# Optimization experiments

Hardware: AMD Instinct MI355X
Metric: run time of the kernel (lower is better)

The kernel has to match this reference:

```python
import jax, jax.numpy as jnp
import numpy as np

B, T, E = 2, 2048, 1024
H = 16
D = E // H  # head_dim = 64


def setup_inputs() -> dict:
    key = jax.random.key(0)
    k1, k2, k3 = jax.random.split(key, 3)
    x = jax.random.normal(k1, (B, T, E), dtype=jnp.float32)
    w_qkv = jax.random.normal(k2, (3 * E, E), dtype=jnp.float32) * 0.02
    w_proj = jax.random.normal(k3, (E, E), dtype=jnp.float32) * 0.02
    return {"x": x, "w_qkv": w_qkv, "w_proj": w_proj}


def reference(x, w_qkv, w_proj):
    b, t, c = x.shape
    # qkv projection (torch Linear: x @ W^T), split into q,k,v
    qkv = jnp.einsum('btc,fc->btf', x, w_qkv)  # [B,T,3E]
    q, k, v = jnp.split(qkv, 3, axis=-1)
    # [B,T,E] -> [B,H,T,D]
    q = q.reshape(b, t, H, D).transpose(0, 2, 1, 3)
    k = k.reshape(b, t, H, D).transpose(0, 2, 1, 3)
    v = v.reshape(b, t, H, D).transpose(0, 2, 1, 3)
    scale = 1.0 / jnp.sqrt(jnp.float32(D))
    att = jnp.einsum('bhqd,bhkd->bhqk', q, k) * scale  # [B,H,T,T]
    causal = jnp.tril(jnp.ones((t, t), dtype=bool))
    att = jnp.where(causal[None, None], att, -jnp.inf)
    att = jax.nn.softmax(att, axis=-1)
    out = jnp.einsum('bhqk,bhkd->bhqd', att, v)  # [B,H,T,D]
    out = out.transpose(0, 2, 1, 3).reshape(b, t, c)  # [B,T,E]
    out = jnp.einsum('btc,oc->bto', out, w_proj)
    return out
```

## Files before the change

### kernel.cpp

```cpp
#include <hip/hip_runtime.h>
#include <stdint.h>
#include <stddef.h>

typedef __attribute__((ext_vector_type(8))) short s16x8;
typedef __attribute__((ext_vector_type(4))) short s16x4;
typedef __attribute__((ext_vector_type(4))) float f32x4;

#define B_  2
#define T_  2048
#define E_  1024
#define H_  16
#define E3_ 3072

__device__ __forceinline__ short f2bf(float f) {
  union { float f; uint32_t u; } v; v.f = f;
  uint32_t u = v.u;
  return (short)((u + 0x7FFFu + ((u >> 16) & 1u)) >> 16);
}

__device__ __forceinline__ uint32_t fbits(float f) {
  union { float f; uint32_t u; } v; v.f = f; return v.u;
}

__device__ __forceinline__ void gload_lds16(const short* g, short* l) {
  __builtin_amdgcn_global_load_lds(
      (__attribute__((address_space(1))) void*)(const_cast<short*>(g)),
      (__attribute__((address_space(3))) void*)(l), 16, 0, 0);
}

__global__ void castk_all(const float* __restrict__ x, const float* __restrict__ wqkv,
                          const float* __restrict__ wproj, short* __restrict__ xb,
                          short* __restrict__ wqkvb, short* __restrict__ wprojb) {
  const int bid = blockIdx.x;
  const float* in; short* out; int i; float sc = 1.0f;
  if (bid < 4096)      { in = x;     out = xb;     i = bid * 256 + threadIdx.x; }
  else if (bid < 7168) { in = wqkv;  out = wqkvb;  i = (bid - 4096) * 256 + threadIdx.x;
                         if (i < 262144) sc = 0.18033688011112042f; }
  else                 { in = wproj; out = wprojb; i = (bid - 7168) * 256 + threadIdx.x; }
  const float4 v = ((const float4*)in)[i];
  s16x4 o;
  o[0] = f2bf(v.x * sc); o[1] = f2bf(v.y * sc);
  o[2] = f2bf(v.z * sc); o[3] = f2bf(v.w * sc);
  ((s16x4*)out)[i] = o;
}

template <int MODE>
__global__ void gemm_nt_128(const short* __restrict__ A, const short* __restrict__ B,
                            void* __restrict__ Cv, short* __restrict__ vt,
                            int M, int N, int K) {
  __shared__ short As[128 * 32];
  __shared__ short Bs[128 * 32];
  const int tid  = threadIdx.x;
  const int lane = tid & 63;
  const int w    = tid >> 6;
  const int quad = lane >> 4;
  const int l16  = lane & 15;
  const int wm   = (w >> 1) * 64;
  const int wn   = (w & 1) * 64;
  const int bm   = blockIdx.y * 128;
  const int bn   = blockIdx.x * 128;

  f32x4 acc[4][4];
#pragma unroll
  for (int i = 0; i < 4; i++)
#pragma unroll
    for (int j = 0; j < 4; j++) acc[i][j] = (f32x4){0.f, 0.f, 0.f, 0.f};

  const int srow = w * 32 + (lane >> 2);
  const int scol = (lane & 3) * 8;
  const short* gA = A + (size_t)(bm + srow) * K + scol;
  const short* gB = B + (size_t)(bn + srow) * K + scol;
  short* lA = As + (w * 32) * 32;
  short* lB = Bs + (w * 32) * 32;

  for (int k0 = 0; k0 < K; k0 += 32) {
    __syncthreads();
    gload_lds16(gA + k0,          lA);
    gload_lds16(gA + 16 * K + k0, lA + 16 * 32);
    gload_lds16(gB + k0,          lB);
    gload_lds16(gB + 16 * K + k0, lB + 16 * 32);
    __syncthreads();

    s16x8 a[4], b[4];
#pragma unroll
    for (int i = 0; i < 4; i++)
      a[i] = *(const s16x8*)&As[(wm + i * 16 + l16) * 32 + quad * 8];
#pragma unroll
    for (int j = 0; j < 4; j++)
      b[j] = *(const s16x8*)&Bs[(wn + j * 16 + l16) * 32 + quad * 8];
#pragma unroll
    for (int i = 0; i < 4; i++)
#pragma unroll
      for (int j = 0; j < 4; j++)
        acc[i][j] = __builtin_amdgcn_mfma_f32_16x16x32_bf16(a[i], b[j], acc[i][j], 0, 0, 0);
  }

  if (MODE == 2 && bn >= 2 * E_) {
#pragma unroll
    for (int i = 0; i < 4; i++) {
      const int token = bm + wm + i * 16 + quad * 4;
      const int bb = token >> 11, t = token & (T_ - 1);
#pragma unroll
      for (int j = 0; j < 4; j++) {
        const int col = bn + wn + j * 16 + l16 - 2 * E_;
        s16x4 pk;
#pragma unroll
        for (int r = 0; r < 4; r++) pk[r] = f2bf(acc[i][j][r]);
        *(s16x4*)&vt[((size_t)(bb * H_ + (col >> 6)) * 64 + (col & 63)) * T_ + t] = pk;
      }
    }
  } else {
#pragma unroll
    for (int i = 0; i < 4; i++) {
      const int row0 = bm + wm + i * 16 + quad * 4;
#pragma unroll
      for (int j = 0; j < 4; j++) {
        const int col = bn + wn + j * 16 + l16;
#pragma unroll
        for (int r = 0; r < 4; r++) {
          const size_t idx = (size_t)(row0 + r) * N + col;
          if (MODE == 2) ((short*)Cv)[idx] = f2bf(acc[i][j][r]);
          else           ((float*)Cv)[idx] = acc[i][j][r];
        }
      }
    }
  }
}

__global__ void __launch_bounds__(128, 2)
attn_kernel(const short* __restrict__ qkv, const short* __restrict__ vt,
            short* __restrict__ attout) {
  __shared__ short Ks[2][64 * 64];
  __shared__ short Vs[2][64 * 64];
  __shared__ short Ps[2][32 * 64];
  const int tid  = threadIdx.x;
  const int lane = tid & 63;
  const int w    = tid >> 6;
  const int quad = lane >> 4;
  const int l16  = lane & 15;
  const int bh = blockIdx.x;
  const int b = bh >> 4, h = bh & 15;
  const int ya = blockIdx.y & 7, yb = blockIdx.y >> 3;
  const int qt = yb * 8 + ((yb & 1) ? (7 - ya) : ya);
  const int q0b = qt * 64;
  const float NEG_INF = -__builtin_inff();

  const int srl = lane >> 3;
  const int sgc = ((lane & 7) ^ srl) * 8;
  const short* gK = qkv + (size_t)(b * T_) * E3_ + E_ + h * 64 + sgc;
  const short* gV = vt + (size_t)(bh * 64) * T_ + sgc;
  const int swz = (l16 & 7);

  s16x8 ones;
#pragma unroll
  for (int i = 0; i < 8; i++) ones[i] = (short)0x3F80;

  auto stage = [&](int kv0s, int bf) {
#pragma unroll
    for (int i = 0; i < 4; i++) {
      const int row = w * 32 + i * 8 + srl;
      gload_lds16(gK + (size_t)(kv0s + row) * E3_, &Ks[bf][(w * 32 + i * 8) * 64]);
      gload_lds16(gV + (size_t)row * T_ + kv0s,    &Vs[bf][(w * 32 + i * 8) * 64]);
    }
  };

  s16x8 qf[2][2];
#pragma unroll
  for (int sub = 0; sub < 2; sub++) {
    const short* qbase = qkv + (size_t)(b * T_ + q0b + w * 32 + sub * 16 + l16) * E3_ + h * 64 + quad * 8;
    qf[sub][0] = *(const s16x8*)(qbase);
    qf[sub][1] = *(const s16x8*)(qbase + 32);
  }

  f32x4 o[2][4], ol[2];
#pragma unroll
  for (int sub = 0; sub < 2; sub++) {
    ol[sub] = (f32x4){0.f, 0.f, 0.f, 0.f};
#pragma unroll
    for (int j = 0; j < 4; j++) o[sub][j] = (f32x4){0.f, 0.f, 0.f, 0.f};
  }

  stage(0, 0);
  __syncthreads();

  for (int kv0 = 0, g = 0; kv0 <= q0b; kv0 += 64, g++) {
    const int cur = g & 1;

    if (kv0 + 64 <= q0b) stage(kv0 + 64, cur ^ 1);

    f32x4 s[2][4];
#pragma unroll
    for (int sub = 0; sub < 2; sub++)
#pragma unroll
      for (int j = 0; j < 4; j++) s[sub][j] = (f32x4){0.f, 0.f, 0.f, 0.f};

    __builtin_amdgcn_s_setprio(1);
#pragma unroll
    for (int c = 0; c < 2; c++) {
      s16x8 kf[4];
#pragma unroll
      for (int j = 0; j < 4; j++)
        kf[j] = *(const s16x8*)&Ks[cur][(j * 16 + l16) * 64 + (((c * 4 + quad) ^ swz) * 8)];
#pragma unroll
      for (int sub = 0; sub < 2; sub++)
#pragma unroll
        for (int j = 0; j < 4; j++)
          s[sub][j] = __builtin_amdgcn_mfma_f32_16x16x32_bf16(kf[j], qf[sub][c], s[sub][j], 0, 0, 0);
    }
    __builtin_amdgcn_s_setprio(0);

    if (kv0 == q0b) {
#pragma unroll
      for (int sub = 0; sub < 2; sub++)
#pragma unroll
        for (int j = 0; j < 4; j++)
#pragma unroll
          for (int r = 0; r < 4; r++)
            if (j * 16 + quad * 4 + r > w * 32 + sub * 16 + l16) s[sub][j][r] = NEG_INF;
    }

#pragma unroll
    for (int sub = 0; sub < 2; sub++)
#pragma unroll
      for (int j = 0; j < 4; j++) {
        const float p0 = exp2f(s[sub][j][0]);
        const float p1 = exp2f(s[sub][j][1]);
        const float p2 = exp2f(s[sub][j][2]);
        const float p3 = exp2f(s[sub][j][3]);
        int2 pk;
        pk.x = (int)__builtin_amdgcn_perm(fbits(p1), fbits(p0), 0x07060302u);
        pk.y = (int)__builtin_amdgcn_perm(fbits(p3), fbits(p2), 0x07060302u);
        short* pw = &Ps[w][(sub * 16 + l16) * 64 + (((2 * j + (quad >> 1)) ^ swz) * 8) + (quad & 1) * 4];
        *(int2*)pw = pk;
      }
    __asm volatile("s_waitcnt lgkmcnt(0)" ::: "memory");

    __builtin_amdgcn_s_setprio(1);
#pragma unroll
    for (int c = 0; c < 2; c++) {
      s16x8 vf[4];
#pragma unroll
      for (int j = 0; j < 4; j++)
        vf[j] = *(const s16x8*)&Vs[cur][(j * 16 + l16) * 64 + (((c * 4 + quad) ^ swz) * 8)];
#pragma unroll
      for (int sub = 0; sub < 2; sub++) {
        const s16x8 pf = *(const s16x8*)&Ps[w][(sub * 16 + l16) * 64 + (((4 * c + quad) ^ swz) * 8)];
        ol[sub] = __builtin_amdgcn_mfma_f32_16x16x32_bf16(pf, ones, ol[sub], 0, 0, 0);
#pragma unroll
        for (int j = 0; j < 4; j++)
          o[sub][j] = __builtin_amdgcn_mfma_f32_16x16x32_bf16(pf, vf[j], o[sub][j], 0, 0, 0);
      }
    }
    __builtin_amdgcn_s_setprio(0);

    __syncthreads();
  }

#pragma unroll
  for (int sub = 0; sub < 2; sub++)
#pragma unroll
    for (int r = 0; r < 4; r++) {
      const float inv = 1.0f / ol[sub][r];
      const int q = q0b + w * 32 + sub * 16 + quad * 4 + r;
      short* ob = attout + ((size_t)(b * T_ + q) * H_ + h) * 64 + l16;
      ob[0]  = f2bf(o[sub][0][r] * inv);
      ob[16] = f2bf(o[sub][1][r] * inv);
      ob[32] = f2bf(o[sub][2][r] * inv);
      ob[48] = f2bf(o[sub][3][r] * inv);
    }
}

extern "C" void kernel_launch(void* const* d_in, const int* in_sizes, int n_in,
                              void* d_out, int out_size, void* d_ws, size_t ws_size,
                              hipStream_t stream) {
  const float* x     = (const float*)d_in[0];
  const float* wqkv  = (const float*)d_in[1];
  const float* wproj = (const float*)d_in[2];

  if (ws_size < 58720256u) return;
  short* ws     = (short*)d_ws;
  short* xb     = ws;
  short* wqkvb  = xb + 4194304;
  short* wprojb = wqkvb + 3145728;
  short* qkv    = wprojb + 1048576;
  short* vt     = qkv + 12582912;
  short* attb   = vt + 4194304;

  castk_all<<<8192, 256, 0, stream>>>(x, wqkv, wproj, xb, wqkvb, wprojb);
  gemm_nt_128<2><<<dim3(24, 32), 256, 0, stream>>>(xb, wqkvb, qkv, vt, 4096, 3072, 1024);
  attn_kernel<<<dim3(32, 32), 128, 0, stream>>>(qkv, vt, attb);
  gemm_nt_128<0><<<dim3(8, 32), 256, 0, stream>>>(attb, wprojb, d_out, nullptr, 4096, 1024, 1024);
}
```

Before: 189.6 us.

## Use 128-row query tiles with four warps and triple-buffered KV staging

New measurement: 187.4 us. Within noise of the previous version (-1.2%).

```diff
diff --git a/kernel.cpp b/kernel.cpp
--- a/kernel.cpp
+++ b/kernel.cpp
@@ -127,12 +127,12 @@
   }
 }
 
-__global__ void __launch_bounds__(128, 2)
+__global__ void __launch_bounds__(256, 2)
 attn_kernel(const short* __restrict__ qkv, const short* __restrict__ vt,
             short* __restrict__ attout) {
-  __shared__ short Ks[2][64 * 64];
-  __shared__ short Vs[2][64 * 64];
-  __shared__ short Ps[2][32 * 64];
+  __shared__ short Ks[3][64 * 64];
+  __shared__ short Vs[3][64 * 64];
+  __shared__ short Ps[4][32 * 64];
   const int tid  = threadIdx.x;
   const int lane = tid & 63;
   const int w    = tid >> 6;
@@ -140,9 +140,10 @@
   const int l16  = lane & 15;
   const int bh = blockIdx.x;
   const int b = bh >> 4, h = bh & 15;
-  const int ya = blockIdx.y & 7, yb = blockIdx.y >> 3;
-  const int qt = yb * 8 + ((yb & 1) ? (7 - ya) : ya);
-  const int q0b = qt * 64;
+  const int y  = blockIdx.y;
+  const int QT = (y < 8) ? y : (23 - y);
+  const int q0b   = QT * 128;
+  const int kvmax = q0b + 64;
   const float NEG_INF = -__builtin_inff();
 
   const int srl = lane >> 3;
@@ -157,10 +158,10 @@
 
   auto stage = [&](int kv0s, int bf) {
 #pragma unroll
-    for (int i = 0; i < 4; i++) {
-      const int row = w * 32 + i * 8 + srl;
-      gload_lds16(gK + (size_t)(kv0s + row) * E3_, &Ks[bf][(w * 32 + i * 8) * 64]);
-      gload_lds16(gV + (size_t)row * T_ + kv0s,    &Vs[bf][(w * 32 + i * 8) * 64]);
+    for (int i = 0; i < 2; i++) {
+      const int r8 = w * 16 + i * 8;
+      gload_lds16(gK + (size_t)(kv0s + r8 + srl) * E3_, &Ks[bf][r8 * 64]);
+      gload_lds16(gV + (size_t)(r8 + srl) * T_ + kv0s,  &Vs[bf][r8 * 64]);
     }
   };
 
@@ -181,79 +182,90 @@
   }
 
   stage(0, 0);
-  __syncthreads();
-
-  for (int kv0 = 0, g = 0; kv0 <= q0b; kv0 += 64, g++) {
-    const int cur = g & 1;
-
-    if (kv0 + 64 <= q0b) stage(kv0 + 64, cur ^ 1);
-
-    f32x4 s[2][4];
-#pragma unroll
-    for (int sub = 0; sub < 2; sub++)
-#pragma unroll
-      for (int j = 0; j < 4; j++) s[sub][j] = (f32x4){0.f, 0.f, 0.f, 0.f};
-
-    __builtin_amdgcn_s_setprio(1);
-#pragma unroll
-    for (int c = 0; c < 2; c++) {
-      s16x8 kf[4];
-#pragma unroll
-      for (int j = 0; j < 4; j++)
-        kf[j] = *(const s16x8*)&Ks[cur][(j * 16 + l16) * 64 + (((c * 4 + quad) ^ swz) * 8)];
+  stage(64, 1);
+
+  const int wq    = (w & 1) * 32;
+  const int wlast = q0b + (w >> 1) * 64;
+
+  int cur = 0, nx2 = 2;
+#pragma unroll 1
+  for (int kv0 = 0; kv0 <= kvmax; kv0 += 64) {
+    if (kv0 < kvmax) __asm volatile("s_waitcnt vmcnt(4)" ::: "memory");
+    else             __asm volatile("s_waitcnt vmcnt(0)" ::: "memory");
+    __builtin_amdgcn_s_barrier();
+    __builtin_amdgcn_sched_barrier(0);
+
+    if (kv0 + 128 <= kvmax) stage(kv0 + 128, nx2);
+
+    if (kv0 <= wlast) {
+      f32x4 s[2][4];
 #pragma unroll
       for (int sub = 0; sub < 2; sub++)
 #pragma unroll
+        for (int j = 0; j < 4; j++) s[sub][j] = (f32x4){0.f, 0.f, 0.f, 0.f};
+
+      __builtin_amdgcn_s_setprio(1);
+#pragma unroll
+      for (int c = 0; c < 2; c++) {
+        s16x8 kf[4];
+#pragma unroll
         for (int j = 0; j < 4; j++)
-          s[sub][j] = __builtin_amdgcn_mfma_f32_16x16x32_bf16(kf[j], qf[sub][c], s[sub][j], 0, 0, 0);
-    }
-    __builtin_amdgcn_s_setprio(0);
-
-    if (kv0 == q0b) {
+          kf[j] = *(const s16x8*)&Ks[cur][(j * 16 + l16) * 64 + (((c * 4 + quad) ^ swz) * 8)];
+#pragma unroll
+        for (int sub = 0; sub < 2; sub++)
+#pragma unroll
+          for (int j = 0; j < 4; j++)
+            s[sub][j] = __builtin_amdgcn_mfma_f32_16x16x32_bf16(kf[j], qf[sub][c], s[sub][j], 0, 0, 0);
+      }
+      __builtin_amdgcn_s_setprio(0);
+
+      if (kv0 == wlast) {
+#pragma unroll
+        for (int sub = 0; sub < 2; sub++)
+#pragma unroll
+          for (int j = 0; j < 4; j++)
+#pragma unroll
+            for (int r = 0; r < 4; r++)
+              if (j * 16 + quad * 4 + r > wq + sub * 16 + l16) s[sub][j][r] = NEG_INF;
+      }
+
 #pragma unroll
       for (int sub = 0; sub < 2; sub++)
 #pragma unroll
+        for (int j = 0; j < 4; j++) {
+          const float p0 = exp2f(s[sub][j][0]);
+          const float p1 = exp2f(s[sub][j][1]);
+          const float p2 = exp2f(s[sub][j][2]);
+          const float p3 = exp2f(s[sub][j][3]);
+          int2 pk;
+          pk.x = (int)__builtin_amdgcn_perm(fbits(p1), fbits(p0), 0x07060302u);
+          pk.y = (int)__builtin_amdgcn_perm(fbits(p3), fbits(p2), 0x07060302u);
+          short* pw = &Ps[w][(sub * 16 + l16) * 64 + (((2 * j + (quad >> 1)) ^ swz) * 8) + (quad & 1) * 4];
+          *(int2*)pw = pk;
+        }
+      __asm volatile("s_waitcnt lgkmcnt(0)" ::: "memory");
+
+      __builtin_amdgcn_s_setprio(1);
+#pragma unroll
+      for (int c = 0; c < 2; c++) {
+        s16x8 vf[4];
+#pragma unroll
         for (int j = 0; j < 4; j++)
-#pragma unroll
-          for (int r = 0; r < 4; r++)
-            if (j * 16 + quad * 4 + r > w * 32 + sub * 16 + l16) s[sub][j][r] = NEG_INF;
-    }
-
-#pragma unroll
-    for (int sub = 0; sub < 2; sub++)
-#pragma unroll
-      for (int j = 0; j < 4; j++) {
-        const float p0 = exp2f(s[sub][j][0]);
-        const float p1 = exp2f(s[sub][j][1]);
-        const float p2 = exp2f(s[sub][j][2]);
-        const float p3 = exp2f(s[sub][j][3]);
-        int2 pk;
-        pk.x = (int)__builtin_amdgcn_perm(fbits(p1), fbits(p0), 0x07060302u);
-        pk.y = (int)__builtin_amdgcn_perm(fbits(p3), fbits(p2), 0x07060302u);
-        short* pw = &Ps[w][(sub * 16 + l16) * 64 + (((2 * j + (quad >> 1)) ^ swz) * 8) + (quad & 1) * 4];
-        *(int2*)pw = pk;
-      }
-    __asm volatile("s_waitcnt lgkmcnt(0)" ::: "memory");
-
-    __builtin_amdgcn_s_setprio(1);
-#pragma unroll
-    for (int c = 0; c < 2; c++) {
-      s16x8 vf[4];
-#pragma unroll
-      for (int j = 0; j < 4; j++)
-        vf[j] = *(const s16x8*)&Vs[cur][(j * 16 + l16) * 64 + (((c * 4 + quad) ^ swz) * 8)];
-#pragma unroll
-      for (int sub = 0; sub < 2; sub++) {
-        const s16x8 pf = *(const s16x8*)&Ps[w][(sub * 16 + l16) * 64 + (((4 * c + quad) ^ swz) * 8)];
-        ol[sub] = __builtin_amdgcn_mfma_f32_16x16x32_bf16(pf, ones, ol[sub], 0, 0, 0);
-#pragma unroll
-        for (int j = 0; j < 4; j++)
-          o[sub][j] = __builtin_amdgcn_mfma_f32_16x16x32_bf16(pf, vf[j], o[sub][j], 0, 0, 0);
-      }
-    }
-    __builtin_amdgcn_s_setprio(0);
-
-    __syncthreads();
+          vf[j] = *(const s16x8*)&Vs[cur][(j * 16 + l16) * 64 + (((c * 4 + quad) ^ swz) * 8)];
+#pragma unroll
+        for (int sub = 0; sub < 2; sub++) {
+          const s16x8 pf = *(const s16x8*)&Ps[w][(sub * 16 + l16) * 64 + (((4 * c + quad) ^ swz) * 8)];
+          ol[sub] = __builtin_amdgcn_mfma_f32_16x16x32_bf16(pf, ones, ol[sub], 0, 0, 0);
+#pragma unroll
+          for (int j = 0; j < 4; j++)
+            o[sub][j] = __builtin_amdgcn_mfma_f32_16x16x32_bf16(pf, vf[j], o[sub][j], 0, 0, 0);
+        }
+      }
+      __builtin_amdgcn_s_setprio(0);
+    }
+
+    cur = (cur == 2) ? 0 : cur + 1;
+    nx2 = (nx2 == 2) ? 0 : nx2 + 1;
   }
 
 #pragma unroll
@@ -288,6 +300,6 @@
 
   castk_all<<<8192, 256, 0, stream>>>(x, wqkv, wproj, xb, wqkvb, wprojb);
   gemm_nt_128<2><<<dim3(24, 32), 256, 0, stream>>>(xb, wqkvb, qkv, vt, 4096, 3072, 1024);
-  attn_kernel<<<dim3(32, 32), 128, 0, stream>>>(qkv, vt, attb);
+  attn_kernel<<<dim3(32, 16), 256, 0, stream>>>(qkv, vt, attb);
   gemm_nt_128<0><<<dim3(8, 32), 256, 0, stream>>>(attb, wprojb, d_out, nullptr, 4096, 1024, 1024);
 }
```

## Split long causal attention rows across blocks and keep P in registers

Applied to the files above, without the earlier changes.

After: 176.1 us. -7.1%, faster.

```diff
diff --git a/kernel.cpp b/kernel.cpp
--- a/kernel.cpp
+++ b/kernel.cpp
@@ -16,10 +16,6 @@
   union { float f; uint32_t u; } v; v.f = f;
   uint32_t u = v.u;
   return (short)((u + 0x7FFFu + ((u >> 16) & 1u)) >> 16);
-}
-
-__device__ __forceinline__ uint32_t fbits(float f) {
-  union { float f; uint32_t u; } v; v.f = f; return v.u;
 }
 
 __device__ __forceinline__ void gload_lds16(const short* g, short* l) {
@@ -127,22 +123,31 @@
   }
 }
 
-__global__ void __launch_bounds__(128, 2)
-attn_kernel(const short* __restrict__ qkv, const short* __restrict__ vt,
-            short* __restrict__ attout) {
+__device__ const unsigned char itab[24] = {
+  0x1F, 0x07, 0x1E, 0x2E, 0x2D, 0x2C, 0x06, 0x2B,
+  0x2F, 0x1D, 0x1C, 0x1A, 0x2A, 0x1B, 0x19, 0x05,
+  0x00, 0x01, 0x02, 0x03, 0x18, 0x28, 0x29, 0x04
+};
+
+__global__ void __launch_bounds__(256, 3)
+attn_kernel(short* qkv, const short* __restrict__ vt,
+            short* __restrict__ attout, float* __restrict__ scr) {
   __shared__ short Ks[2][64 * 64];
   __shared__ short Vs[2][64 * 64];
-  __shared__ short Ps[2][32 * 64];
   const int tid  = threadIdx.x;
   const int lane = tid & 63;
   const int w    = tid >> 6;
   const int quad = lane >> 4;
   const int l16  = lane & 15;
-  const int bh = blockIdx.x;
+  const int bh = blockIdx.x & 31;
   const int b = bh >> 4, h = bh & 15;
-  const int ya = blockIdx.y & 7, yb = blockIdx.y >> 3;
-  const int qt = yb * 8 + ((yb & 1) ? (7 - ya) : ya);
-  const int q0b = qt * 64;
+  const int e = itab[blockIdx.x >> 5];
+  const int Q = e & 15, kind = e >> 4;
+  const int t0 = (kind == 2) ? (Q + 1) : 0;
+  const int t1 = (kind == 1) ? Q : (2 * Q + 1);
+  const int q0w = Q * 128 + w * 32;
+  const int tp  = 2 * Q + (w >> 1);
+  const int woff = (w & 1) * 32;
   const float NEG_INF = -__builtin_inff();
 
   const int srl = lane >> 3;
@@ -157,17 +162,19 @@
 
   auto stage = [&](int kv0s, int bf) {
 #pragma unroll
-    for (int i = 0; i < 4; i++) {
-      const int row = w * 32 + i * 8 + srl;
-      gload_lds16(gK + (size_t)(kv0s + row) * E3_, &Ks[bf][(w * 32 + i * 8) * 64]);
-      gload_lds16(gV + (size_t)row * T_ + kv0s,    &Vs[bf][(w * 32 + i * 8) * 64]);
+    for (int i = 0; i < 2; i++) {
+      const int r8 = w * 16 + i * 8;
+      const int rowp = r8 + srl;
+      const int rowk = (rowp & ~12) | ((rowp & 4) << 1) | ((rowp & 8) >> 1);
+      gload_lds16(gK + (size_t)(kv0s + rowk) * E3_, &Ks[bf][r8 * 64]);
+      gload_lds16(gV + (size_t)rowp * T_ + kv0s,    &Vs[bf][r8 * 64]);
     }
   };
 
   s16x8 qf[2][2];
 #pragma unroll
   for (int sub = 0; sub < 2; sub++) {
-    const short* qbase = qkv + (size_t)(b * T_ + q0b + w * 32 + sub * 16 + l16) * E3_ + h * 64 + quad * 8;
+    const short* qbase = qkv + (size_t)(b * T_ + q0w + sub * 16 + l16) * E3_ + h * 64 + quad * 8;
     qf[sub][0] = *(const s16x8*)(qbase);
     qf[sub][1] = *(const s16x8*)(qbase + 32);
   }
@@ -180,94 +187,141 @@
     for (int j = 0; j < 4; j++) o[sub][j] = (f32x4){0.f, 0.f, 0.f, 0.f};
   }
 
-  stage(0, 0);
+  stage(t0 * 64, 0);
   __syncthreads();
 
-  for (int kv0 = 0, g = 0; kv0 <= q0b; kv0 += 64, g++) {
-    const int cur = g & 1;
-
-    if (kv0 + 64 <= q0b) stage(kv0 + 64, cur ^ 1);
-
-    f32x4 s[2][4];
-#pragma unroll
-    for (int sub = 0; sub < 2; sub++)
-#pragma unroll
-      for (int j = 0; j < 4; j++) s[sub][j] = (f32x4){0.f, 0.f, 0.f, 0.f};
-
-    __builtin_amdgcn_s_setprio(1);
-#pragma unroll
-    for (int c = 0; c < 2; c++) {
-      s16x8 kf[4];
-#pragma unroll
-      for (int j = 0; j < 4; j++)
-        kf[j] = *(const s16x8*)&Ks[cur][(j * 16 + l16) * 64 + (((c * 4 + quad) ^ swz) * 8)];
+#pragma unroll 1
+  for (int t = t0; t <= t1; t++) {
+    const int cur = (t - t0) & 1;
+    if (t + 1 <= t1) stage((t + 1) * 64, cur ^ 1);
+
+    if (t <= tp) {
+      f32x4 s[2][4];
 #pragma unroll
       for (int sub = 0; sub < 2; sub++)
 #pragma unroll
+        for (int j = 0; j < 4; j++) s[sub][j] = (f32x4){0.f, 0.f, 0.f, 0.f};
+
+      __builtin_amdgcn_s_setprio(1);
+#pragma unroll
+      for (int c = 0; c < 2; c++) {
+        s16x8 kf[4];
+#pragma unroll
         for (int j = 0; j < 4; j++)
-          s[sub][j] = __builtin_amdgcn_mfma_f32_16x16x32_bf16(kf[j], qf[sub][c], s[sub][j], 0, 0, 0);
-    }
-    __builtin_amdgcn_s_setprio(0);
-
-    if (kv0 == q0b) {
-#pragma unroll
-      for (int sub = 0; sub < 2; sub++)
+          kf[j] = *(const s16x8*)&Ks[cur][(j * 16 + l16) * 64 + (((c * 4 + quad) ^ swz) * 8)];
+#pragma unroll
+        for (int sub = 0; sub < 2; sub++)
+#pragma unroll
+          for (int j = 0; j < 4; j++)
+            s[sub][j] = __builtin_amdgcn_mfma_f32_16x16x32_bf16(kf[j], qf[sub][c], s[sub][j], 0, 0, 0);
+      }
+      __builtin_amdgcn_s_setprio(0);
+
+      if (t == tp) {
+        const int tq4 = ((quad & 1) << 3) | ((quad >> 1) << 2);
+#pragma unroll
+        for (int sub = 0; sub < 2; sub++)
+#pragma unroll
+          for (int j = 0; j < 4; j++)
+#pragma unroll
+            for (int r = 0; r < 4; r++)
+              if (j * 16 + tq4 + r > woff + sub * 16 + l16) s[sub][j][r] = NEG_INF;
+      }
+
+      s16x8 F[2][2];
+#pragma unroll
+      for (int sub = 0; sub < 2; sub++) {
+#pragma unroll
+        for (int j = 0; j < 4; j++) {
+          s[sub][j][0] = exp2f(s[sub][j][0]); s[sub][j][1] = exp2f(s[sub][j][1]);
+          s[sub][j][2] = exp2f(s[sub][j][2]); s[sub][j][3] = exp2f(s[sub][j][3]);
+        }
+#pragma unroll
+        for (int c = 0; c < 2; c++) {
+          int x0, x1, y0, y1;
+          asm("v_cvt_pk_bf16_f32 %0, %1, %2" : "=v"(x0) : "v"(s[sub][2 * c][0]), "v"(s[sub][2 * c][1]));
+          asm("v_cvt_pk_bf16_f32 %0, %1, %2" : "=v"(x1) : "v"(s[sub][2 * c][2]), "v"(s[sub][2 * c][3]));
+          asm("v_cvt_pk_bf16_f32 %0, %1, %2" : "=v"(y0) : "v"(s[sub][2 * c + 1][0]), "v"(s[sub][2 * c + 1][1]));
+          asm("v_cvt_pk_bf16_f32 %0, %1, %2" : "=v"(y1) : "v"(s[sub][2 * c + 1][2]), "v"(s[sub][2 * c + 1][3]));
+          asm("v_permlane32_swap_b32 %0, %1" : "+v"(x0), "+v"(y0));
+          asm("v_permlane32_swap_b32 %0, %1" : "+v"(x1), "+v"(y1));
+          union { int i4[4]; s16x8 v; } u;
+          u.i4[0] = x0; u.i4[1] = x1; u.i4[2] = y0; u.i4[3] = y1;
+          F[sub][c] = u.v;
+        }
+      }
+
+      __builtin_amdgcn_s_setprio(1);
+#pragma unroll
+      for (int c = 0; c < 2; c++) {
+        s16x8 vf[4];
 #pragma unroll
         for (int j = 0; j < 4; j++)
-#pragma unroll
-          for (int r = 0; r < 4; r++)
-            if (j * 16 + quad * 4 + r > w * 32 + sub * 16 + l16) s[sub][j][r] = NEG_INF;
-    }
-
-#pragma unroll
-    for (int sub = 0; sub < 2; sub++)
+          vf[j] = *(const s16x8*)&Vs[cur][(j * 16 + l16) * 64 + (((c * 4 + quad) ^ swz) * 8)];
+#pragma unroll
+        for (int sub = 0; sub < 2; sub++) {
+          ol[sub] = __builtin_amdgcn_mfma_f32_16x16x32_bf16(ones, F[sub][c], ol[sub], 0, 0, 0);
+#pragma unroll
+          for (int j = 0; j < 4; j++)
+            o[sub][j] = __builtin_amdgcn_mfma_f32_16x16x32_bf16(vf[j], F[sub][c], o[sub][j], 0, 0, 0);
+        }
+      }
+      __builtin_amdgcn_s_setprio(0);
+    }
+
+    __syncthreads();
+  }
+
+  if (kind == 0) {
+#pragma unroll
+    for (int sub = 0; sub < 2; sub++) {
+      const float inv = 1.0f / ol[sub][0];
+      const int q = q0w + sub * 16 + l16;
+      short* ob = attout + ((size_t)(b * T_ + q) * H_ + h) * 64 + quad * 4;
 #pragma unroll
       for (int j = 0; j < 4; j++) {
-        const float p0 = exp2f(s[sub][j][0]);
-        const float p1 = exp2f(s[sub][j][1]);
-        const float p2 = exp2f(s[sub][j][2]);
-        const float p3 = exp2f(s[sub][j][3]);
-        int2 pk;
-        pk.x = (int)__builtin_amdgcn_perm(fbits(p1), fbits(p0), 0x07060302u);
-        pk.y = (int)__builtin_amdgcn_perm(fbits(p3), fbits(p2), 0x07060302u);
-        short* pw = &Ps[w][(sub * 16 + l16) * 64 + (((2 * j + (quad >> 1)) ^ swz) * 8) + (quad & 1) * 4];
-        *(int2*)pw = pk;
-      }
-    __asm volatile("s_waitcnt lgkmcnt(0)" ::: "memory");
-
-    __builtin_amdgcn_s_setprio(1);
-#pragma unroll
-    for (int c = 0; c < 2; c++) {
-      s16x8 vf[4];
-#pragma unroll
-      for (int j = 0; j < 4; j++)
-        vf[j] = *(const s16x8*)&Vs[cur][(j * 16 + l16) * 64 + (((c * 4 + quad) ^ swz) * 8)];
-#pragma unroll
-      for (int sub = 0; sub < 2; sub++) {
-        const s16x8 pf = *(const s16x8*)&Ps[w][(sub * 16 + l16) * 64 + (((4 * c + quad) ^ swz) * 8)];
-        ol[sub] = __builtin_amdgcn_mfma_f32_16x16x32_bf16(pf, ones, ol[sub], 0, 0, 0);
-#pragma unroll
-        for (int j = 0; j < 4; j++)
-          o[sub][j] = __builtin_amdgcn_mfma_f32_16x16x32_bf16(pf, vf[j], o[sub][j], 0, 0, 0);
-      }
-    }
-    __builtin_amdgcn_s_setprio(0);
-
-    __syncthreads();
-  }
-
-#pragma unroll
-  for (int sub = 0; sub < 2; sub++)
-#pragma unroll
-    for (int r = 0; r < 4; r++) {
-      const float inv = 1.0f / ol[sub][r];
-      const int q = q0b + w * 32 + sub * 16 + quad * 4 + r;
-      short* ob = attout + ((size_t)(b * T_ + q) * H_ + h) * 64 + l16;
-      ob[0]  = f2bf(o[sub][0][r] * inv);
-      ob[16] = f2bf(o[sub][1][r] * inv);
-      ob[32] = f2bf(o[sub][2][r] * inv);
-      ob[48] = f2bf(o[sub][3][r] * inv);
-    }
+        s16x4 pk;
+#pragma unroll
+        for (int r = 0; r < 4; r++) pk[r] = f2bf(o[sub][j][r] * inv);
+        *(s16x4*)&ob[16 * j] = pk;
+      }
+    }
+  } else {
+    float* sc = scr + (kind == 2 ? 2097152 : 0);
+#pragma unroll
+    for (int sub = 0; sub < 2; sub++) {
+      const int q = q0w + sub * 16 + l16;
+      const int qi = q - 1024;
+      float* sp = sc + ((size_t)(bh * 1024 + qi)) * 64 + quad * 4;
+#pragma unroll
+      for (int j = 0; j < 4; j++) *(f32x4*)&sp[16 * j] = o[sub][j];
+      if (quad == 0) {
+        float* lp = (float*)(qkv + (size_t)(b * T_ + q) * E3_ + 2 * E_);
+        lp[h + (kind == 2 ? 16 : 0)] = ol[sub][0];
+      }
+    }
+  }
+}
+
+__global__ void att_norm(const float* __restrict__ scr, const short* __restrict__ qkv,
+                         short* __restrict__ attb) {
+  const int bid = blockIdx.x;
+  const int bh2 = bid & 31;
+  const int g   = bid >> 5;
+  const int tid = threadIdx.x;
+  const int qi  = g * 16 + (tid >> 4);
+  const int d0  = (tid & 15) * 4;
+  const int b = bh2 >> 4, h = bh2 & 15;
+  const size_t idx = ((size_t)bh2 * 1024 + qi) * 64 + d0;
+  const f32x4 a = *(const f32x4*)&scr[idx];
+  const f32x4 c = *(const f32x4*)&scr[2097152 + idx];
+  const float* lp = (const float*)(qkv + (size_t)(b * T_ + 1024 + qi) * E3_ + 2 * E_);
+  const float inv = 1.0f / (lp[h] + lp[16 + h]);
+  short* ob = attb + ((size_t)(b * T_ + 1024 + qi) * H_ + h) * 64 + d0;
+  s16x4 pk;
+#pragma unroll
+  for (int r = 0; r < 4; r++) pk[r] = f2bf((a[r] + c[r]) * inv);
+  *(s16x4*)ob = pk;
 }
 
 extern "C" void kernel_launch(void* const* d_in, const int* in_sizes, int n_in,
@@ -288,6 +342,7 @@
 
   castk_all<<<8192, 256, 0, stream>>>(x, wqkv, wproj, xb, wqkvb, wprojb);
   gemm_nt_128<2><<<dim3(24, 32), 256, 0, stream>>>(xb, wqkvb, qkv, vt, 4096, 3072, 1024);
-  attn_kernel<<<dim3(32, 32), 128, 0, stream>>>(qkv, vt, attb);
+  attn_kernel<<<dim3(768), 256, 0, stream>>>(qkv, vt, attb, (float*)d_out);
+  att_norm<<<dim3(2048), 256, 0, stream>>>((const float*)d_out, qkv, attb);
   gemm_nt_128<0><<<dim3(8, 32), 256, 0, stream>>>(attb, wprojb, d_out, nullptr, 4096, 1024, 1024);
 }
```
